# Kernel optimization log

Hardware: AMD Instinct MI355X
Metric: run time of the kernel (lower is better)

## Reference

```python
import jax, jax.numpy as jnp
import numpy as np

WIDTH = 1024
N_HEADS = 16
EPS = 1e-5


def _layernorm(x, gamma, beta):
    m = jnp.mean(x, axis=-1, keepdims=True)
    v = jnp.mean((x - m) ** 2, axis=-1, keepdims=True)  # unbiased=False
    return (x - m) / jnp.sqrt(v + EPS) * gamma + beta


def setup_inputs() -> dict:
    key = jax.random.key(0)
    ks = jax.random.split(key, 8)
    d = WIDTH
    x = jax.random.normal(ks[0], (4, 1024, d), dtype=jnp.float32)
    # MHA params (torch.rand -> uniform [0,1); scale down for numerical sanity is NOT
    # done in the original, but uniform init matches torch.rand semantics)
    in_project = jax.random.uniform(ks[1], (3 * d, d), dtype=jnp.float32)
    out_project = jax.random.uniform(ks[2], (d, d), dtype=jnp.float32)
    ln1_gamma = jnp.ones((d,), jnp.float32)
    ln1_beta = jnp.zeros((d,), jnp.float32)
    ln2_gamma = jnp.ones((d,), jnp.float32)
    ln2_beta = jnp.zeros((d,), jnp.float32)
    w_up = jax.random.uniform(ks[3], (d, 2 * d), dtype=jnp.float32)
    b_up = jax.random.uniform(ks[4], (2 * d,), dtype=jnp.float32)
    w_down = jax.random.uniform(ks[5], (2 * d, d), dtype=jnp.float32)
    b_down = jax.random.uniform(ks[6], (d,), dtype=jnp.float32)
    return {"x": x, "in_project": in_project, "out_project": out_project,
            "ln1_gamma": ln1_gamma, "ln1_beta": ln1_beta,
            "w_up": w_up, "b_up": b_up, "w_down": w_down, "b_down": b_down,
            "ln2_gamma": ln2_gamma, "ln2_beta": ln2_beta}


def reference(x, in_project, out_project, ln1_gamma, ln1_beta,
              w_up, b_up, w_down, b_down, ln2_gamma, ln2_beta):
    B, S, d = x.shape
    H = N_HEADS
    dh = d // H

    # --- masked_attention(ln_1(x)), attn_mask is None ---
    h = _layernorm(x, ln1_gamma, ln1_beta)
    qkv = h @ in_project.T                       # [B,S,3d]
    qkv = qkv.reshape(B, S, 3, H, dh)            # 3H axis splits as (3, H)
    q, k, v = qkv[:, :, 0], qkv[:, :, 1], qkv[:, :, 2]   # [B,S,H,dh]
    scores = jnp.einsum('bqhd,bkhd->bhqk', q, k) / jnp.sqrt(jnp.float32(dh))
    attn = jax.nn.softmax(scores, axis=-1)       # materialized [B,H,S,S] as in original
    o = jnp.einsum('bhqk,bkhd->bqhd', attn, v).reshape(B, S, d)
    o = o @ out_project                          # note: NOT transposed in original
    x = x + o

    # --- ff(ln_2(x)) ---
    h2 = _layernorm(x, ln2_gamma, ln2_beta)
    ff = jnp.maximum(h2 @ w_up + b_up, 0.0) @ w_down + b_down
    return x + ff
```

## Files before the change

### kernel.cpp

```cpp
#include <hip/hip_runtime.h>
#include <hip/hip_bf16.h>


typedef short bf16x8 __attribute__((ext_vector_type(8)));
typedef float f32x4 __attribute__((ext_vector_type(4)));
typedef float f32x16 __attribute__((ext_vector_type(16)));

__device__ __forceinline__ unsigned short f2bf(float f) {
  unsigned int u = __float_as_uint(f);
  unsigned int r = (u + 0x7fffu + ((u >> 16) & 1u)) >> 16;
  return (unsigned short)r;
}
__device__ __forceinline__ float bf2f(unsigned short h) {
  return __uint_as_float(((unsigned int)h) << 16);
}
__device__ __forceinline__ unsigned pack2t(float x, float y) {
  return __builtin_amdgcn_perm(__float_as_uint(y), __float_as_uint(x),
                               0x07060302u);
}
__device__ __forceinline__ float fexp2(float x) {
#if defined(__has_builtin)
#if __has_builtin(__builtin_amdgcn_exp2f)
  return __builtin_amdgcn_exp2f(x);
#else
  return exp2f(x);
#endif
#else
  return exp2f(x);
#endif
}

__device__ __forceinline__ void gld16(const void* g, void* l) {
  __builtin_amdgcn_global_load_lds(
      (const __attribute__((address_space(1))) unsigned int*)g,
      (__attribute__((address_space(3))) unsigned int*)l, 16, 0, 0);
}

#if defined(__has_builtin)
#if __has_builtin(__builtin_amdgcn_permlane32_swap)
#define HAVE_PLSWAP 1
#endif
#endif

__device__ __forceinline__ void plswap(unsigned& a, unsigned& b) {
#ifdef HAVE_PLSWAP
  auto r = __builtin_amdgcn_permlane32_swap(a, b, 0, 0);
  a = r[0];
  b = r[1];
#else
  unsigned ta = (unsigned)__shfl_xor((int)a, 32);
  unsigned tb = (unsigned)__shfl_xor((int)b, 32);
  bool hi = (threadIdx.x & 32) != 0;
  unsigned na = hi ? tb : a;
  unsigned nb = hi ? b : ta;
  a = na;
  b = nb;
#endif
}


__global__ __launch_bounds__(256) void prep_kernel(
    const float* __restrict__ x, const float* __restrict__ g1,
    const float* __restrict__ b1, unsigned short* __restrict__ h_hi,
    unsigned short* __restrict__ h_lo, const float* __restrict__ in_project,
    unsigned short* __restrict__ Wq_hi, unsigned short* __restrict__ Wq_lo,
    const float* __restrict__ op, const float* __restrict__ wu,
    const float* __restrict__ wd, unsigned short* __restrict__ oT,
    unsigned short* __restrict__ uT, unsigned short* __restrict__ dT) {
  __shared__ float t[32][33];
  __shared__ float red[8];
  const int blk = blockIdx.x;
  const int tid = threadIdx.x;

  if (blk < 4096) {
    const int row = blk;
    float4 v = ((const float4*)x)[(size_t)row * 256 + tid];
    float s = v.x + v.y + v.z + v.w;
    float ss = v.x * v.x + v.y * v.y + v.z * v.z + v.w * v.w;
#pragma unroll
    for (int off = 32; off; off >>= 1) {
      s += __shfl_xor(s, off);
      ss += __shfl_xor(ss, off);
    }
    int wid = tid >> 6, lane = tid & 63;
    if (lane == 0) { red[wid] = s; red[4 + wid] = ss; }
    __syncthreads();
    s = red[0] + red[1] + red[2] + red[3];
    ss = red[4] + red[5] + red[6] + red[7];
    float mean = s * (1.f / 1024.f);
    float var = ss * (1.f / 1024.f) - mean * mean;
    float inv = rsqrtf(var + 1e-5f);
    float4 g = ((const float4*)g1)[tid];
    float4 bt = ((const float4*)b1)[tid];
    float y[4];
    y[0] = (v.x - mean) * inv * g.x + bt.x;
    y[1] = (v.y - mean) * inv * g.y + bt.y;
    y[2] = (v.z - mean) * inv * g.z + bt.z;
    y[3] = (v.w - mean) * inv * g.w + bt.w;
    size_t o = (size_t)row * 1024 + tid * 4;
#pragma unroll
    for (int j = 0; j < 4; ++j) {
      unsigned short hb = f2bf(y[j]);
      h_hi[o + j] = hb;
      h_lo[o + j] = f2bf(y[j] - bf2f(hb));
    }
  } else if (blk < 9216) {
    const float* in;
    unsigned short* out;
    int R, C, bc, br;
    if (blk < 5120) {
      int i2 = blk - 4096;
      in = op; out = oT; R = 1024; C = 1024;
      bc = (i2 & 31) << 5; br = (i2 >> 5) << 5;
    } else if (blk < 7168) {
      int i2 = blk - 5120;
      in = wu; out = uT; R = 1024; C = 2048;
      bc = (i2 & 63) << 5; br = (i2 >> 6) << 5;
    } else {
      int i2 = blk - 7168;
      in = wd; out = dT; R = 2048; C = 1024;
      bc = (i2 & 31) << 5; br = (i2 >> 5) << 5;
    }
    const int tx = tid & 31, ty = tid >> 5;
#pragma unroll
    for (int i = ty; i < 32; i += 8)
      t[i][tx] = in[(size_t)(br + i) * C + bc + tx];
    __syncthreads();
#pragma unroll
    for (int i = ty; i < 32; i += 8)
      out[(size_t)(bc + i) * R + br + tx] = f2bf(t[tx][i]);
  } else {
    const int n = 3072 * 1024;
    int i = (blk - 9216) * 256 + tid;
    for (; i < n; i += 1024 * 256) {
      float v = in_project[i];
      unsigned short h = f2bf(v);
      Wq_hi[i] = h;
      Wq_lo[i] = f2bf(v - bf2f(h));
    }
  }
}


__global__ __launch_bounds__(256) void ln2_kernel(
    const float* __restrict__ x, const float* __restrict__ gamma,
    const float* __restrict__ beta, unsigned short* __restrict__ hi) {
  int row = blockIdx.x, tid = threadIdx.x;
  float4 v = ((const float4*)x)[(size_t)row * 256 + tid];
  float s = v.x + v.y + v.z + v.w;
  float ss = v.x * v.x + v.y * v.y + v.z * v.z + v.w * v.w;
#pragma unroll
  for (int off = 32; off; off >>= 1) {
    s += __shfl_xor(s, off);
    ss += __shfl_xor(ss, off);
  }
  __shared__ float red[8];
  int wid = tid >> 6, lane = tid & 63;
  if (lane == 0) { red[wid] = s; red[4 + wid] = ss; }
  __syncthreads();
  s = red[0] + red[1] + red[2] + red[3];
  ss = red[4] + red[5] + red[6] + red[7];
  float mean = s * (1.f / 1024.f);
  float var = ss * (1.f / 1024.f) - mean * mean;
  float inv = rsqrtf(var + 1e-5f);
  float4 g = ((const float4*)gamma)[tid];
  float4 bt = ((const float4*)beta)[tid];
  size_t o = (size_t)row * 1024 + tid * 4;
  hi[o + 0] = f2bf((v.x - mean) * inv * g.x + bt.x);
  hi[o + 1] = f2bf((v.y - mean) * inv * g.y + bt.y);
  hi[o + 2] = f2bf((v.z - mean) * inv * g.z + bt.z);
  hi[o + 3] = f2bf((v.w - mean) * inv * g.w + bt.w);
}


template <bool SPLIT, bool BIAS, bool RESID, bool RELU, bool OUTBF16,
          int OUTMODE>
__global__ __launch_bounds__(256) void gemm_kernel(
    const short* __restrict__ Ah, const short* __restrict__ Al,
    const short* __restrict__ Bh, const short* __restrict__ Bl,
    const float* __restrict__ bias, const float* __restrict__ resid,
    void* __restrict__ outp, int M, int N, int K,
    unsigned short* __restrict__ qh, unsigned short* __restrict__ ql,
    unsigned short* __restrict__ kh, unsigned short* __restrict__ kl,
    unsigned short* __restrict__ vtp) {
  __shared__ short As[2][128 * 32];
  __shared__ short Bs[2][128 * 32];
  __shared__ short As2[SPLIT ? 2 : 1][SPLIT ? 128 * 32 : 8];
  __shared__ short Bs2[SPLIT ? 2 : 1][SPLIT ? 128 * 32 : 8];

  const int tid = threadIdx.x;
  const int lane = tid & 63;
  const int wid = tid >> 6;
  const int wr = (wid >> 1) << 6;
  const int wc = (wid & 1) << 6;
  const int l15 = lane & 15, lh = lane >> 4;
  const int rowBase = blockIdx.y << 7;
  const int colBase = blockIdx.x << 7;

  const int sr = tid >> 2;
  const int sc = (tid & 3) << 3;
  const int soff = sr * 32 + sc;
  const short* Ag = Ah + (size_t)(rowBase + sr) * K + sc;
  const short* Bg = Bh + (size_t)(colBase + sr) * K + sc;
  const short* Ag2 = SPLIT ? Al + (size_t)(rowBase + sr) * K + sc : nullptr;
  const short* Bg2 = SPLIT ? Bl + (size_t)(colBase + sr) * K + sc : nullptr;

  f32x4 acc[4][4];
#pragma unroll
  for (int m = 0; m < 4; ++m)
#pragma unroll
    for (int n = 0; n < 4; ++n) acc[m][n] = (f32x4){0.f, 0.f, 0.f, 0.f};

  const int kT = K >> 5;
  {
    gld16(Ag, &As[0][soff]);
    gld16(Ag + (size_t)64 * K, &As[0][soff + 64 * 32]);
    gld16(Bg, &Bs[0][soff]);
    gld16(Bg + (size_t)64 * K, &Bs[0][soff + 64 * 32]);
    if constexpr (SPLIT) {
      gld16(Ag2, &As2[0][soff]);
      gld16(Ag2 + (size_t)64 * K, &As2[0][soff + 64 * 32]);
      gld16(Bg2, &Bs2[0][soff]);
      gld16(Bg2 + (size_t)64 * K, &Bs2[0][soff + 64 * 32]);
    }
  }

  for (int kt = 0; kt < kT; ++kt) {
    __syncthreads();
    const int cb = kt & 1;
    if (kt + 1 < kT) {
      const int nb = cb ^ 1;
      const int k0 = (kt + 1) << 5;
      gld16(Ag + k0, &As[nb][soff]);
      gld16(Ag + k0 + (size_t)64 * K, &As[nb][soff + 64 * 32]);
      gld16(Bg + k0, &Bs[nb][soff]);
      gld16(Bg + k0 + (size_t)64 * K, &Bs[nb][soff + 64 * 32]);
      if constexpr (SPLIT) {
        gld16(Ag2 + k0, &As2[nb][soff]);
        gld16(Ag2 + k0 + (size_t)64 * K, &As2[nb][soff + 64 * 32]);
        gld16(Bg2 + k0, &Bs2[nb][soff]);
        gld16(Bg2 + k0 + (size_t)64 * K, &Bs2[nb][soff + 64 * 32]);
      }
    }

    const short* Asb = As[cb];
    const short* Bsb = Bs[cb];
    bf16x8 af[4], bfr[4];
#pragma unroll
    for (int m = 0; m < 4; ++m)
      af[m] = *(const bf16x8*)&Asb[(wr + m * 16 + l15) * 32 + lh * 8];
#pragma unroll
    for (int n = 0; n < 4; ++n)
      bfr[n] = *(const bf16x8*)&Bsb[(wc + n * 16 + l15) * 32 + lh * 8];
    if constexpr (SPLIT) {
      const short* Asb2 = As2[cb];
      const short* Bsb2 = Bs2[cb];
      bf16x8 af2[4], bfr2[4];
#pragma unroll
      for (int m = 0; m < 4; ++m)
        af2[m] = *(const bf16x8*)&Asb2[(wr + m * 16 + l15) * 32 + lh * 8];
#pragma unroll
      for (int n = 0; n < 4; ++n)
        bfr2[n] = *(const bf16x8*)&Bsb2[(wc + n * 16 + l15) * 32 + lh * 8];
#pragma unroll
      for (int m = 0; m < 4; ++m)
#pragma unroll
        for (int n = 0; n < 4; ++n) {
          acc[m][n] = __builtin_amdgcn_mfma_f32_16x16x32_bf16(af[m], bfr[n], acc[m][n], 0, 0, 0);
          acc[m][n] = __builtin_amdgcn_mfma_f32_16x16x32_bf16(af[m], bfr2[n], acc[m][n], 0, 0, 0);
          acc[m][n] = __builtin_amdgcn_mfma_f32_16x16x32_bf16(af2[m], bfr[n], acc[m][n], 0, 0, 0);
        }
    } else {
#pragma unroll
      for (int m = 0; m < 4; ++m)
#pragma unroll
        for (int n = 0; n < 4; ++n)
          acc[m][n] = __builtin_amdgcn_mfma_f32_16x16x32_bf16(af[m], bfr[n], acc[m][n], 0, 0, 0);
    }
  }

  const int prow = rowBase + wr + lh * 4;
  const int pcol = colBase + wc + l15;
#pragma unroll
  for (int m = 0; m < 4; ++m) {
#pragma unroll
    for (int n = 0; n < 4; ++n) {
      const int c = pcol + n * 16;
      if constexpr (OUTMODE == 2) {
        const int head = c >> 6, dim = c & 63;
        const int r0_ = prow + m * 16;
        const int b = r0_ >> 10, s0 = r0_ & 1023;
        unsigned lo = ((unsigned)f2bf(acc[m][n][1]) << 16) | f2bf(acc[m][n][0]);
        unsigned hi2 = ((unsigned)f2bf(acc[m][n][3]) << 16) | f2bf(acc[m][n][2]);
        unsigned long long wv = ((unsigned long long)hi2 << 32) | lo;
        *(unsigned long long*)&vtp[(((size_t)(b * 16 + head)) * 64 + dim) * 1024 + s0] = wv;
      } else {
        float badd = 0.f;
        if constexpr (BIAS) badd = bias[c];
#pragma unroll
        for (int i = 0; i < 4; ++i) {
          const int r = prow + m * 16 + i;
          float v = acc[m][n][i] + badd;
          if constexpr (OUTMODE == 1) {
            const int part = c >> 10;
            const int cc = c & 1023;
            const int head = cc >> 6, dim = cc & 63;
            const int b = r >> 10, s = r & 1023;
            size_t idx = (((size_t)(b * 16 + head)) * 1024 + s) * 64 + dim;
            if (part == 0) {
              float y = v * 0.18033688f;
              unsigned short hb = f2bf(y);
              qh[idx] = hb;
              ql[idx] = f2bf(y - bf2f(hb));
            } else {
              unsigned short hb = f2bf(v);
              kh[idx] = hb;
              kl[idx] = f2bf(v - bf2f(hb));
            }
          } else {
            if constexpr (RESID) v += resid[(size_t)r * N + c];
            if constexpr (RELU) v = fmaxf(v, 0.f);
            if constexpr (OUTBF16)
              ((unsigned short*)outp)[(size_t)r * N + c] = f2bf(v);
            else
              ((float*)outp)[(size_t)r * N + c] = v;
          }
        }
      }
    }
  }
}


__global__ __launch_bounds__(256, 3) void attn_mfma_kernel(
    const short* __restrict__ qhi, const short* __restrict__ qlo,
    const short* __restrict__ khi, const short* __restrict__ klo,
    const short* __restrict__ vt, unsigned short* __restrict__ o,
    int S, int H) {
  __shared__ short Kh[2][64 * 64];
  __shared__ short Kl[2][64 * 64];
  __shared__ short Vs[2][64 * 64];

  const int tid = threadIdx.x, lane = tid & 63, wid = tid >> 6;
  const int l31 = lane & 31;
  const int hi = lane >> 5;
  const int blk = blockIdx.x;
  const int j = blk >> 3;
  const int bh = ((blk & 7) << 3) + (j & 7);
  const int q0 = (j >> 3) << 7;
  const size_t hbase = (size_t)bh * S * 64;

  const size_t qrow = hbase + (size_t)(q0 + wid * 32 + l31) * 64;
  bf16x8 qfh[4], qfl[4];
#pragma unroll
  for (int t = 0; t < 4; ++t) {
    qfh[t] = *(const bf16x8*)(qhi + qrow + t * 16 + hi * 8);
    qfl[t] = *(const bf16x8*)(qlo + qrow + t * 16 + hi * 8);
  }

  float m_run = -INFINITY, l_run = 0.f;
  f32x16 accO0, accO1;
#pragma unroll
  for (int r = 0; r < 16; ++r) { accO0[r] = 0.f; accO1[r] = 0.f; }

  const int r0 = tid >> 3, c0 = tid & 7;
  const int sw0 = ((c0 ^ (r0 & 7)) << 3);
  const int r1 = r0 + 32;
  const int sw1 = ((c0 ^ (r1 & 7)) << 3);

  const int nT = S >> 6;
  {
    gld16(khi + hbase + r0 * 64 + sw0, (char*)Kh[0] + tid * 16);
    gld16(khi + hbase + r1 * 64 + sw1, (char*)Kh[0] + tid * 16 + 4096);
    gld16(klo + hbase + r0 * 64 + sw0, (char*)Kl[0] + tid * 16);
    gld16(klo + hbase + r1 * 64 + sw1, (char*)Kl[0] + tid * 16 + 4096);
    gld16(vt + hbase + (size_t)r0 * S + sw0, (char*)Vs[0] + tid * 16);
    gld16(vt + hbase + (size_t)r1 * S + sw1, (char*)Vs[0] + tid * 16 + 4096);
  }

  for (int kt = 0; kt < nT; ++kt) {
    __syncthreads();
    const int cb = kt & 1;
    if (kt + 1 < nT) {
      const int nb = cb ^ 1;
      const size_t kb = hbase + (size_t)(kt + 1) * 64 * 64;
      gld16(khi + kb + r0 * 64 + sw0, (char*)Kh[nb] + tid * 16);
      gld16(khi + kb + r1 * 64 + sw1, (char*)Kh[nb] + tid * 16 + 4096);
      gld16(klo + kb + r0 * 64 + sw0, (char*)Kl[nb] + tid * 16);
      gld16(klo + kb + r1 * 64 + sw1, (char*)Kl[nb] + tid * 16 + 4096);
      const short* vg = vt + hbase + (size_t)(kt + 1) * 64;
      gld16(vg + (size_t)r0 * S + sw0, (char*)Vs[nb] + tid * 16);
      gld16(vg + (size_t)r1 * S + sw1, (char*)Vs[nb] + tid * 16 + 4096);
    }

    const short* KhB = Kh[cb];
    const short* KlB = Kl[cb];
    const short* VsB = Vs[cb];

    f32x16 sA, sB, sA2, sB2;
#pragma unroll
    for (int r = 0; r < 16; ++r) { sA[r] = 0.f; sB[r] = 0.f; sA2[r] = 0.f; sB2[r] = 0.f; }
    __builtin_amdgcn_s_setprio(1);
#pragma unroll
    for (int t = 0; t < 4; ++t) {
      const int cA = ((2 * t + hi) ^ (l31 & 7)) << 3;
      bf16x8 kh0 = *(const bf16x8*)&KhB[l31 * 64 + cA];
      bf16x8 kl0 = *(const bf16x8*)&KlB[l31 * 64 + cA];
      bf16x8 kh1 = *(const bf16x8*)&KhB[(32 + l31) * 64 + cA];
      bf16x8 kl1 = *(const bf16x8*)&KlB[(32 + l31) * 64 + cA];
      f32x16& dA = (t < 2) ? sA : sA2;
      f32x16& dB = (t < 2) ? sB : sB2;
      dA = __builtin_amdgcn_mfma_f32_32x32x16_bf16(kh0, qfh[t], dA, 0, 0, 0);
      dB = __builtin_amdgcn_mfma_f32_32x32x16_bf16(kh1, qfh[t], dB, 0, 0, 0);
      dA = __builtin_amdgcn_mfma_f32_32x32x16_bf16(kh0, qfl[t], dA, 0, 0, 0);
      dB = __builtin_amdgcn_mfma_f32_32x32x16_bf16(kh1, qfl[t], dB, 0, 0, 0);
      dA = __builtin_amdgcn_mfma_f32_32x32x16_bf16(kl0, qfh[t], dA, 0, 0, 0);
      dB = __builtin_amdgcn_mfma_f32_32x32x16_bf16(kl1, qfh[t], dB, 0, 0, 0);
    }
    __builtin_amdgcn_s_setprio(0);
#pragma unroll
    for (int r = 0; r < 16; ++r) { sA[r] += sA2[r]; sB[r] += sB2[r]; }

    float t8[8];
#pragma unroll
    for (int r = 0; r < 8; ++r)
      t8[r] = fmaxf(fmaxf(sA[2 * r], sA[2 * r + 1]),
                    fmaxf(sB[2 * r], sB[2 * r + 1]));
    float t4a = fmaxf(t8[0], t8[1]), t4b = fmaxf(t8[2], t8[3]);
    float t4c = fmaxf(t8[4], t8[5]), t4d = fmaxf(t8[6], t8[7]);
    float mt = fmaxf(fmaxf(t4a, t4b), fmaxf(t4c, t4d));
    {
      unsigned ma = __float_as_uint(mt), mb = ma;
      plswap(ma, mb);
      mt = fmaxf(__uint_as_float(ma), __uint_as_float(mb));
    }

    if (__any(mt > m_run + 11.5f)) {
      float mn = fmaxf(m_run, mt);
      float a = fexp2(m_run - mn);
      m_run = mn;
      l_run *= a;
#pragma unroll
      for (int r = 0; r < 16; ++r) {
        const int qq = (r & 3) + 8 * (r >> 2) + 4 * hi;
        float ar = __shfl(a, qq);
        accO0[r] *= ar;
        accO1[r] *= ar;
      }
    }

    float ls = 0.f;
#pragma unroll
    for (int r = 0; r < 16; ++r) {
      sA[r] = fexp2(sA[r] - m_run);
      sB[r] = fexp2(sB[r] - m_run);
      ls += sA[r] + sB[r];
    }
    l_run += ls;

    unsigned a0 = pack2t(sA[0], sA[1]), a1 = pack2t(sA[2], sA[3]);
    unsigned a2 = pack2t(sA[4], sA[5]), a3 = pack2t(sA[6], sA[7]);
    plswap(a0, a2);
    plswap(a1, a3);
    unsigned b0 = pack2t(sA[8], sA[9]), b1 = pack2t(sA[10], sA[11]);
    unsigned b2 = pack2t(sA[12], sA[13]), b3 = pack2t(sA[14], sA[15]);
    plswap(b0, b2);
    plswap(b1, b3);
    unsigned c0_ = pack2t(sB[0], sB[1]), c1_ = pack2t(sB[2], sB[3]);
    unsigned c2_ = pack2t(sB[4], sB[5]), c3_ = pack2t(sB[6], sB[7]);
    plswap(c0_, c2_);
    plswap(c1_, c3_);
    unsigned d0 = pack2t(sB[8], sB[9]), d1 = pack2t(sB[10], sB[11]);
    unsigned d2 = pack2t(sB[12], sB[13]), d3 = pack2t(sB[14], sB[15]);
    plswap(d0, d2);
    plswap(d1, d3);

    bf16x8 pf0, pf1, pf2, pf3;
    {
      unsigned w[4];
      w[0] = a0; w[1] = a1; w[2] = a2; w[3] = a3;
      pf0 = *(bf16x8*)w;
      w[0] = b0; w[1] = b1; w[2] = b2; w[3] = b3;
      pf1 = *(bf16x8*)w;
      w[0] = c0_; w[1] = c1_; w[2] = c2_; w[3] = c3_;
      pf2 = *(bf16x8*)w;
      w[0] = d0; w[1] = d1; w[2] = d2; w[3] = d3;
      pf3 = *(bf16x8*)w;
    }

    __builtin_amdgcn_s_setprio(1);
    {
      const int d1r = 32 + l31;
#pragma unroll
      for (int c = 0; c < 4; ++c) {
        bf16x8 bv0 = *(const bf16x8*)&VsB[l31 * 64 + ((((2 * c + hi)) ^ (l31 & 7)) << 3)];
        bf16x8 bv1 = *(const bf16x8*)&VsB[d1r * 64 + ((((2 * c + hi)) ^ (d1r & 7)) << 3)];
        bf16x8 pf = (c == 0) ? pf0 : (c == 1) ? pf1 : (c == 2) ? pf2 : pf3;
        accO0 = __builtin_amdgcn_mfma_f32_32x32x16_bf16(pf, bv0, accO0, 0, 0, 0);
        accO1 = __builtin_amdgcn_mfma_f32_32x32x16_bf16(pf, bv1, accO1, 0, 0, 0);
      }
    }
    __builtin_amdgcn_s_setprio(0);
  }

  {
    unsigned la = __float_as_uint(l_run), lb = la;
    plswap(la, lb);
    l_run = __uint_as_float(la) + __uint_as_float(lb);
  }
  float lrec = 1.0f / l_run;

  const int b = bh >> 4, h = bh & 15;
#pragma unroll
  for (int r = 0; r < 16; ++r) {
    const int qq = (r & 3) + 8 * (r >> 2) + 4 * hi;
    float rr = __shfl(lrec, qq);
    const size_t row = (size_t)(b * S + q0 + wid * 32 + qq) * 1024 + h * 64;
    o[row + l31] = f2bf(accO0[r] * rr);
    o[row + 32 + l31] = f2bf(accO1[r] * rr);
  }
}


extern "C" void kernel_launch(void* const* d_in, const int* in_sizes, int n_in,
                              void* d_out, int out_size, void* d_ws,
                              size_t ws_size, hipStream_t stream) {
  const float* x = (const float*)d_in[0];
  const float* in_project = (const float*)d_in[1];
  const float* out_project = (const float*)d_in[2];
  const float* ln1_g = (const float*)d_in[3];
  const float* ln1_b = (const float*)d_in[4];
  const float* w_up = (const float*)d_in[5];
  const float* b_up = (const float*)d_in[6];
  const float* w_down = (const float*)d_in[7];
  const float* b_down = (const float*)d_in[8];
  const float* ln2_g = (const float*)d_in[9];
  const float* ln2_b = (const float*)d_in[10];

  const int B = in_sizes[0] / (1024 * 1024);
  const int S = 1024, H = 16;
  const int M = B * S;

  char* ws = (char*)d_ws;
  short* h_hi = (short*)(ws + 0);
  short* h_lo = (short*)(ws + 8388608);
  float* x2 = (float*)(ws + 0);
  short* qhi = (short*)(ws + 16777216);
  short* qlo = (short*)(ws + 25165824);
  short* khi = (short*)(ws + 33554432);
  short* klo = (short*)(ws + 41943040);
  short* vt  = (short*)(ws + 50331648);
  short* o = (short*)(ws + 67108864);
  short* h2 = (short*)(ws + 75497472);
  short* u = (short*)(ws + 83886080);
  short* Wq_hi = (short*)(ws + 100663296);
  short* Wq_lo = (short*)(ws + 106954752);
  short* WoT = (short*)(ws + 113246208);
  short* WupT = (short*)(ws + 115343360);
  short* WdnT = (short*)(ws + 119537664);

  prep_kernel<<<10240, 256, 0, stream>>>(
      x, ln1_g, ln1_b, (unsigned short*)h_hi, (unsigned short*)h_lo,
      in_project, (unsigned short*)Wq_hi, (unsigned short*)Wq_lo,
      out_project, w_up, w_down, (unsigned short*)WoT, (unsigned short*)WupT,
      (unsigned short*)WdnT);

  gemm_kernel<true, false, false, false, false, 1>
      <<<dim3(2048 / 128, M / 128), 256, 0, stream>>>(
          h_hi, h_lo, Wq_hi, Wq_lo, nullptr, nullptr, nullptr, M, 2048, 1024,
          (unsigned short*)qhi, (unsigned short*)qlo, (unsigned short*)khi,
          (unsigned short*)klo, nullptr);

  gemm_kernel<false, false, false, false, false, 2>
      <<<dim3(1024 / 128, M / 128), 256, 0, stream>>>(
          h_hi, nullptr, Wq_hi + (size_t)2048 * 1024, nullptr, nullptr, nullptr,
          nullptr, M, 1024, 1024, nullptr, nullptr, nullptr, nullptr,
          (unsigned short*)vt);

  attn_mfma_kernel<<<512, 256, 0, stream>>>(
      qhi, qlo, khi, klo, vt, (unsigned short*)o, S, H);

  gemm_kernel<false, false, true, false, false, 0>
      <<<dim3(1024 / 128, M / 128), 256, 0, stream>>>(
          o, nullptr, WoT, nullptr, nullptr, x, x2, M, 1024, 1024,
          nullptr, nullptr, nullptr, nullptr, nullptr);

  ln2_kernel<<<M, 256, 0, stream>>>(x2, ln2_g, ln2_b, (unsigned short*)h2);

  gemm_kernel<false, true, false, true, true, 0>
      <<<dim3(2048 / 128, M / 128), 256, 0, stream>>>(
          h2, nullptr, WupT, nullptr, b_up, nullptr, u, M, 2048, 1024,
          nullptr, nullptr, nullptr, nullptr, nullptr);

  gemm_kernel<false, true, true, false, false, 0>
      <<<dim3(1024 / 128, M / 128), 256, 0, stream>>>(
          u, nullptr, WdnT, nullptr, b_down, x2, d_out, M, 1024, 2048,
          nullptr, nullptr, nullptr, nullptr, nullptr);
}
```

Measured before the change: 243.0 us.

## Use 128x64 tiles for N=1024 GEMMs and remap workgroups across XCDs

Adds a template parameter that sets the GEMM's N tile width, and switches the three N=1024 GEMMs to 128x64 tiles. This doubles their grids from 256 to 512 workgroups, so more of the 256 CUs stay busy. It also remaps the linear workgroup index so that consecutive blocks handled by the same XCD cover nearby tiles, which should improve L2 reuse. In exchange, the narrower tiles do less MFMA work per LDS and global load, and the remap assumes the workgroup count divides by 8.

```diff
diff --git a/kernel.cpp b/kernel.cpp
--- a/kernel.cpp
+++ b/kernel.cpp
@@ -174,7 +174,7 @@
 
 
 template <bool SPLIT, bool BIAS, bool RESID, bool RELU, bool OUTBF16,
-          int OUTMODE>
+          int OUTMODE, int BNF>
 __global__ __launch_bounds__(256) void gemm_kernel(
     const short* __restrict__ Ah, const short* __restrict__ Al,
     const short* __restrict__ Bh, const short* __restrict__ Bl,
@@ -183,19 +183,25 @@
     unsigned short* __restrict__ qh, unsigned short* __restrict__ ql,
     unsigned short* __restrict__ kh, unsigned short* __restrict__ kl,
     unsigned short* __restrict__ vtp) {
+  constexpr int BN = BNF * 32;
   __shared__ short As[2][128 * 32];
-  __shared__ short Bs[2][128 * 32];
+  __shared__ short Bs[2][BN * 32];
   __shared__ short As2[SPLIT ? 2 : 1][SPLIT ? 128 * 32 : 8];
-  __shared__ short Bs2[SPLIT ? 2 : 1][SPLIT ? 128 * 32 : 8];
+  __shared__ short Bs2[SPLIT ? 2 : 1][SPLIT ? BN * 32 : 8];
 
   const int tid = threadIdx.x;
   const int lane = tid & 63;
   const int wid = tid >> 6;
   const int wr = (wid >> 1) << 6;
-  const int wc = (wid & 1) << 6;
+  const int wc = (wid & 1) * (BNF * 16);
   const int l15 = lane & 15, lh = lane >> 4;
-  const int rowBase = blockIdx.y << 7;
-  const int colBase = blockIdx.x << 7;
+
+  const int gx = gridDim.x;
+  const int lin = blockIdx.y * gx + blockIdx.x;
+  const int nwg = gx * gridDim.y;
+  const int nl = (lin & 7) * (nwg >> 3) + (lin >> 3);
+  const int rowBase = (nl / gx) << 7;
+  const int colBase = (nl % gx) * BN;
 
   const int sr = tid >> 2;
   const int sc = (tid & 3) << 3;
@@ -205,23 +211,24 @@
   const short* Ag2 = SPLIT ? Al + (size_t)(rowBase + sr) * K + sc : nullptr;
   const short* Bg2 = SPLIT ? Bl + (size_t)(colBase + sr) * K + sc : nullptr;
 
-  f32x4 acc[4][4];
+  f32x4 acc[4][BNF];
 #pragma unroll
   for (int m = 0; m < 4; ++m)
 #pragma unroll
-    for (int n = 0; n < 4; ++n) acc[m][n] = (f32x4){0.f, 0.f, 0.f, 0.f};
+    for (int n = 0; n < BNF; ++n) acc[m][n] = (f32x4){0.f, 0.f, 0.f, 0.f};
 
   const int kT = K >> 5;
   {
     gld16(Ag, &As[0][soff]);
     gld16(Ag + (size_t)64 * K, &As[0][soff + 64 * 32]);
     gld16(Bg, &Bs[0][soff]);
-    gld16(Bg + (size_t)64 * K, &Bs[0][soff + 64 * 32]);
+    if constexpr (BNF == 4) gld16(Bg + (size_t)64 * K, &Bs[0][soff + 64 * 32]);
     if constexpr (SPLIT) {
       gld16(Ag2, &As2[0][soff]);
       gld16(Ag2 + (size_t)64 * K, &As2[0][soff + 64 * 32]);
       gld16(Bg2, &Bs2[0][soff]);
-      gld16(Bg2 + (size_t)64 * K, &Bs2[0][soff + 64 * 32]);
+      if constexpr (BNF == 4)
+        gld16(Bg2 + (size_t)64 * K, &Bs2[0][soff + 64 * 32]);
     }
   }
 
@@ -234,38 +241,40 @@
       gld16(Ag + k0, &As[nb][soff]);
       gld16(Ag + k0 + (size_t)64 * K, &As[nb][soff + 64 * 32]);
       gld16(Bg + k0, &Bs[nb][soff]);
-      gld16(Bg + k0 + (size_t)64 * K, &Bs[nb][soff + 64 * 32]);
+      if constexpr (BNF == 4)
+        gld16(Bg + k0 + (size_t)64 * K, &Bs[nb][soff + 64 * 32]);
       if constexpr (SPLIT) {
         gld16(Ag2 + k0, &As2[nb][soff]);
         gld16(Ag2 + k0 + (size_t)64 * K, &As2[nb][soff + 64 * 32]);
         gld16(Bg2 + k0, &Bs2[nb][soff]);
-        gld16(Bg2 + k0 + (size_t)64 * K, &Bs2[nb][soff + 64 * 32]);
+        if constexpr (BNF == 4)
+          gld16(Bg2 + k0 + (size_t)64 * K, &Bs2[nb][soff + 64 * 32]);
       }
     }
 
     const short* Asb = As[cb];
     const short* Bsb = Bs[cb];
-    bf16x8 af[4], bfr[4];
+    bf16x8 af[4], bfr[BNF];
 #pragma unroll
     for (int m = 0; m < 4; ++m)
       af[m] = *(const bf16x8*)&Asb[(wr + m * 16 + l15) * 32 + lh * 8];
 #pragma unroll
-    for (int n = 0; n < 4; ++n)
+    for (int n = 0; n < BNF; ++n)
       bfr[n] = *(const bf16x8*)&Bsb[(wc + n * 16 + l15) * 32 + lh * 8];
     if constexpr (SPLIT) {
       const short* Asb2 = As2[cb];
       const short* Bsb2 = Bs2[cb];
-      bf16x8 af2[4], bfr2[4];
+      bf16x8 af2[4], bfr2[BNF];
 #pragma unroll
       for (int m = 0; m < 4; ++m)
         af2[m] = *(const bf16x8*)&Asb2[(wr + m * 16 + l15) * 32 + lh * 8];
 #pragma unroll
-      for (int n = 0; n < 4; ++n)
+      for (int n = 0; n < BNF; ++n)
         bfr2[n] = *(const bf16x8*)&Bsb2[(wc + n * 16 + l15) * 32 + lh * 8];
 #pragma unroll
       for (int m = 0; m < 4; ++m)
 #pragma unroll
-        for (int n = 0; n < 4; ++n) {
+        for (int n = 0; n < BNF; ++n) {
           acc[m][n] = __builtin_amdgcn_mfma_f32_16x16x32_bf16(af[m], bfr[n], acc[m][n], 0, 0, 0);
           acc[m][n] = __builtin_amdgcn_mfma_f32_16x16x32_bf16(af[m], bfr2[n], acc[m][n], 0, 0, 0);
           acc[m][n] = __builtin_amdgcn_mfma_f32_16x16x32_bf16(af2[m], bfr[n], acc[m][n], 0, 0, 0);
@@ -274,7 +283,7 @@
 #pragma unroll
       for (int m = 0; m < 4; ++m)
 #pragma unroll
-        for (int n = 0; n < 4; ++n)
+        for (int n = 0; n < BNF; ++n)
           acc[m][n] = __builtin_amdgcn_mfma_f32_16x16x32_bf16(af[m], bfr[n], acc[m][n], 0, 0, 0);
     }
   }
@@ -284,7 +293,7 @@
 #pragma unroll
   for (int m = 0; m < 4; ++m) {
 #pragma unroll
-    for (int n = 0; n < 4; ++n) {
+    for (int n = 0; n < BNF; ++n) {
       const int c = pcol + n * 16;
       if constexpr (OUTMODE == 2) {
         const int head = c >> 6, dim = c & 63;
@@ -565,14 +574,14 @@
       out_project, w_up, w_down, (unsigned short*)WoT, (unsigned short*)WupT,
       (unsigned short*)WdnT);
 
-  gemm_kernel<true, false, false, false, false, 1>
+  gemm_kernel<true, false, false, false, false, 1, 4>
       <<<dim3(2048 / 128, M / 128), 256, 0, stream>>>(
           h_hi, h_lo, Wq_hi, Wq_lo, nullptr, nullptr, nullptr, M, 2048, 1024,
           (unsigned short*)qhi, (unsigned short*)qlo, (unsigned short*)khi,
           (unsigned short*)klo, nullptr);
 
-  gemm_kernel<false, false, false, false, false, 2>
-      <<<dim3(1024 / 128, M / 128), 256, 0, stream>>>(
+  gemm_kernel<false, false, false, false, false, 2, 2>
+      <<<dim3(1024 / 64, M / 128), 256, 0, stream>>>(
           h_hi, nullptr, Wq_hi + (size_t)2048 * 1024, nullptr, nullptr, nullptr,
           nullptr, M, 1024, 1024, nullptr, nullptr, nullptr, nullptr,
           (unsigned short*)vt);
@@ -580,20 +589,20 @@
   attn_mfma_kernel<<<512, 256, 0, stream>>>(
       qhi, qlo, khi, klo, vt, (unsigned short*)o, S, H);
 
-  gemm_kernel<false, false, true, false, false, 0>
-      <<<dim3(1024 / 128, M / 128), 256, 0, stream>>>(
+  gemm_kernel<false, false, true, false, false, 0, 2>
+      <<<dim3(1024 / 64, M / 128), 256, 0, stream>>>(
           o, nullptr, WoT, nullptr, nullptr, x, x2, M, 1024, 1024,
           nullptr, nullptr, nullptr, nullptr, nullptr);
 
   ln2_kernel<<<M, 256, 0, stream>>>(x2, ln2_g, ln2_b, (unsigned short*)h2);
 
-  gemm_kernel<false, true, false, true, true, 0>
+  gemm_kernel<false, true, false, true, true, 0, 4>
       <<<dim3(2048 / 128, M / 128), 256, 0, stream>>>(
           h2, nullptr, WupT, nullptr, b_up, nullptr, u, M, 2048, 1024,
           nullptr, nullptr, nullptr, nullptr, nullptr);
 
-  gemm_kernel<false, true, true, false, false, 0>
-      <<<dim3(1024 / 128, M / 128), 256, 0, stream>>>(
+  gemm_kernel<false, true, true, false, false, 0, 2>
+      <<<dim3(1024 / 64, M / 128), 256, 0, stream>>>(
           u, nullptr, WdnT, nullptr, b_down, x2, d_out, M, 1024, 2048,
           nullptr, nullptr, nullptr, nullptr, nullptr);
 }
```

Result: faster. 228.0 us, median of 2 (-6.2%).

## Add 64x64-tile GEMM for N=1024 projections and swizzle block order

Applied to the files above, without the earlier changes.

Adds a gemm64 kernel with 64x64 output tiles and uses it for the V projection, the output projection and the down projection. With 128x128 tiles these GEMMs launch only 256 workgroups, too few to fill the GPU; 64x64 tiles give 1024. Both GEMM kernels also remap workgroup IDs in groups of eight so that concurrently running blocks share operand tiles in cache. Smaller tiles lower per-block data reuse and raise global and LDS traffic per FLOP.

```diff
diff --git a/kernel.cpp b/kernel.cpp
--- a/kernel.cpp
+++ b/kernel.cpp
@@ -181,8 +181,7 @@
     const float* __restrict__ bias, const float* __restrict__ resid,
     void* __restrict__ outp, int M, int N, int K,
     unsigned short* __restrict__ qh, unsigned short* __restrict__ ql,
-    unsigned short* __restrict__ kh, unsigned short* __restrict__ kl,
-    unsigned short* __restrict__ vtp) {
+    unsigned short* __restrict__ kh, unsigned short* __restrict__ kl) {
   __shared__ short As[2][128 * 32];
   __shared__ short Bs[2][128 * 32];
   __shared__ short As2[SPLIT ? 2 : 1][SPLIT ? 128 * 32 : 8];
@@ -194,8 +193,13 @@
   const int wr = (wid >> 1) << 6;
   const int wc = (wid & 1) << 6;
   const int l15 = lane & 15, lh = lane >> 4;
-  const int rowBase = blockIdx.y << 7;
-  const int colBase = blockIdx.x << 7;
+
+  const int gx = gridDim.x;
+  const int lin = blockIdx.y * gx + blockIdx.x;
+  const int nwg = gx * gridDim.y;
+  const int nl = (lin & 7) * (nwg >> 3) + (lin >> 3);
+  const int rowBase = (nl / gx) << 7;
+  const int colBase = (nl % gx) << 7;
 
   const int sr = tid >> 2;
   const int sc = (tid & 3) << 3;
@@ -286,6 +290,116 @@
 #pragma unroll
     for (int n = 0; n < 4; ++n) {
       const int c = pcol + n * 16;
+      float badd = 0.f;
+      if constexpr (BIAS) badd = bias[c];
+#pragma unroll
+      for (int i = 0; i < 4; ++i) {
+        const int r = prow + m * 16 + i;
+        float v = acc[m][n][i] + badd;
+        if constexpr (OUTMODE == 1) {
+          const int part = c >> 10;
+          const int cc = c & 1023;
+          const int head = cc >> 6, dim = cc & 63;
+          const int b = r >> 10, s = r & 1023;
+          size_t idx = (((size_t)(b * 16 + head)) * 1024 + s) * 64 + dim;
+          if (part == 0) {
+            float y = v * 0.18033688f;
+            unsigned short hb = f2bf(y);
+            qh[idx] = hb;
+            ql[idx] = f2bf(y - bf2f(hb));
+          } else {
+            unsigned short hb = f2bf(v);
+            kh[idx] = hb;
+            kl[idx] = f2bf(v - bf2f(hb));
+          }
+        } else {
+          if constexpr (RESID) v += resid[(size_t)r * N + c];
+          if constexpr (RELU) v = fmaxf(v, 0.f);
+          if constexpr (OUTBF16)
+            ((unsigned short*)outp)[(size_t)r * N + c] = f2bf(v);
+          else
+            ((float*)outp)[(size_t)r * N + c] = v;
+        }
+      }
+    }
+  }
+}
+
+
+template <bool BIAS, bool RESID, bool RELU, bool OUTBF16, int OUTMODE>
+__global__ __launch_bounds__(256) void gemm64_kernel(
+    const short* __restrict__ Ah, const short* __restrict__ Bh,
+    const float* __restrict__ bias, const float* __restrict__ resid,
+    void* __restrict__ outp, int M, int N, int K,
+    unsigned short* __restrict__ vtp) {
+  __shared__ short As[2][64 * 32];
+  __shared__ short Bs[2][64 * 32];
+
+  const int tid = threadIdx.x;
+  const int lane = tid & 63;
+  const int wid = tid >> 6;
+  const int wr = (wid >> 1) << 5;
+  const int wc = (wid & 1) << 5;
+  const int l15 = lane & 15, lh = lane >> 4;
+
+  const int gx = gridDim.x;
+  const int lin = blockIdx.y * gx + blockIdx.x;
+  const int nwg = gx * gridDim.y;
+  const int nl = (lin & 7) * (nwg >> 3) + (lin >> 3);
+  const int rowBase = (nl / gx) << 6;
+  const int colBase = (nl % gx) << 6;
+
+  const int sr = tid >> 2;
+  const int sc = (tid & 3) << 3;
+  const int soff = sr * 32 + sc;
+  const short* Ag = Ah + (size_t)(rowBase + sr) * K + sc;
+  const short* Bg = Bh + (size_t)(colBase + sr) * K + sc;
+
+  f32x4 acc[2][2];
+#pragma unroll
+  for (int m = 0; m < 2; ++m)
+#pragma unroll
+    for (int n = 0; n < 2; ++n) acc[m][n] = (f32x4){0.f, 0.f, 0.f, 0.f};
+
+  const int kT = K >> 5;
+  {
+    gld16(Ag, &As[0][soff]);
+    gld16(Bg, &Bs[0][soff]);
+  }
+
+  for (int kt = 0; kt < kT; ++kt) {
+    __syncthreads();
+    const int cb = kt & 1;
+    if (kt + 1 < kT) {
+      const int nb = cb ^ 1;
+      const int k0 = (kt + 1) << 5;
+      gld16(Ag + k0, &As[nb][soff]);
+      gld16(Bg + k0, &Bs[nb][soff]);
+    }
+
+    const short* Asb = As[cb];
+    const short* Bsb = Bs[cb];
+    bf16x8 af[2], bfr[2];
+#pragma unroll
+    for (int m = 0; m < 2; ++m)
+      af[m] = *(const bf16x8*)&Asb[(wr + m * 16 + l15) * 32 + lh * 8];
+#pragma unroll
+    for (int n = 0; n < 2; ++n)
+      bfr[n] = *(const bf16x8*)&Bsb[(wc + n * 16 + l15) * 32 + lh * 8];
+#pragma unroll
+    for (int m = 0; m < 2; ++m)
+#pragma unroll
+      for (int n = 0; n < 2; ++n)
+        acc[m][n] = __builtin_amdgcn_mfma_f32_16x16x32_bf16(af[m], bfr[n], acc[m][n], 0, 0, 0);
+  }
+
+  const int prow = rowBase + wr + lh * 4;
+  const int pcol = colBase + wc + l15;
+#pragma unroll
+  for (int m = 0; m < 2; ++m) {
+#pragma unroll
+    for (int n = 0; n < 2; ++n) {
+      const int c = pcol + n * 16;
       if constexpr (OUTMODE == 2) {
         const int head = c >> 6, dim = c & 63;
         const int r0_ = prow + m * 16;
@@ -301,30 +415,12 @@
         for (int i = 0; i < 4; ++i) {
           const int r = prow + m * 16 + i;
           float v = acc[m][n][i] + badd;
-          if constexpr (OUTMODE == 1) {
-            const int part = c >> 10;
-            const int cc = c & 1023;
-            const int head = cc >> 6, dim = cc & 63;
-            const int b = r >> 10, s = r & 1023;
-            size_t idx = (((size_t)(b * 16 + head)) * 1024 + s) * 64 + dim;
-            if (part == 0) {
-              float y = v * 0.18033688f;
-              unsigned short hb = f2bf(y);
-              qh[idx] = hb;
-              ql[idx] = f2bf(y - bf2f(hb));
-            } else {
-              unsigned short hb = f2bf(v);
-              kh[idx] = hb;
-              kl[idx] = f2bf(v - bf2f(hb));
-            }
-          } else {
-            if constexpr (RESID) v += resid[(size_t)r * N + c];
-            if constexpr (RELU) v = fmaxf(v, 0.f);
-            if constexpr (OUTBF16)
-              ((unsigned short*)outp)[(size_t)r * N + c] = f2bf(v);
-            else
-              ((float*)outp)[(size_t)r * N + c] = v;
-          }
+          if constexpr (RESID) v += resid[(size_t)r * N + c];
+          if constexpr (RELU) v = fmaxf(v, 0.f);
+          if constexpr (OUTBF16)
+            ((unsigned short*)outp)[(size_t)r * N + c] = f2bf(v);
+          else
+            ((float*)outp)[(size_t)r * N + c] = v;
         }
       }
     }
@@ -569,31 +665,28 @@
       <<<dim3(2048 / 128, M / 128), 256, 0, stream>>>(
           h_hi, h_lo, Wq_hi, Wq_lo, nullptr, nullptr, nullptr, M, 2048, 1024,
           (unsigned short*)qhi, (unsigned short*)qlo, (unsigned short*)khi,
-          (unsigned short*)klo, nullptr);
-
-  gemm_kernel<false, false, false, false, false, 2>
-      <<<dim3(1024 / 128, M / 128), 256, 0, stream>>>(
-          h_hi, nullptr, Wq_hi + (size_t)2048 * 1024, nullptr, nullptr, nullptr,
-          nullptr, M, 1024, 1024, nullptr, nullptr, nullptr, nullptr,
-          (unsigned short*)vt);
+          (unsigned short*)klo);
+
+  gemm64_kernel<false, false, false, false, 2>
+      <<<dim3(1024 / 64, M / 64), 256, 0, stream>>>(
+          h_hi, Wq_hi + (size_t)2048 * 1024, nullptr, nullptr, nullptr,
+          M, 1024, 1024, (unsigned short*)vt);
 
   attn_mfma_kernel<<<512, 256, 0, stream>>>(
       qhi, qlo, khi, klo, vt, (unsigned short*)o, S, H);
 
-  gemm_kernel<false, false, true, false, false, 0>
-      <<<dim3(1024 / 128, M / 128), 256, 0, stream>>>(
-          o, nullptr, WoT, nullptr, nullptr, x, x2, M, 1024, 1024,
-          nullptr, nullptr, nullptr, nullptr, nullptr);
+  gemm64_kernel<false, true, false, false, 0>
+      <<<dim3(1024 / 64, M / 64), 256, 0, stream>>>(
+          o, WoT, nullptr, x, x2, M, 1024, 1024, nullptr);
 
   ln2_kernel<<<M, 256, 0, stream>>>(x2, ln2_g, ln2_b, (unsigned short*)h2);
 
   gemm_kernel<false, true, false, true, true, 0>
       <<<dim3(2048 / 128, M / 128), 256, 0, stream>>>(
           h2, nullptr, WupT, nullptr, b_up, nullptr, u, M, 2048, 1024,
-          nullptr, nullptr, nullptr, nullptr, nullptr);
-
-  gemm_kernel<false, true, true, false, false, 0>
-      <<<dim3(1024 / 128, M / 128), 256, 0, stream>>>(
-          u, nullptr, WdnT, nullptr, b_down, x2, d_out, M, 1024, 2048,
-          nullptr, nullptr, nullptr, nullptr, nullptr);
-}
+          nullptr, nullptr, nullptr, nullptr);
+
+  gemm64_kernel<true, true, false, false, 0>
+      <<<dim3(1024 / 64, M / 64), 256, 0, stream>>>(
+          u, WdnT, b_down, x2, d_out, M, 1024, 2048, nullptr);
+}
```

Measured after the change: 220.9 us, median of 2. -9.1%, faster.
